# Kernel optimization log

Measured on AMD Instinct MI355X. Metric: run time of the kernel, lower is better.

The kernel has to match this reference:

```python
import math
import jax, jax.numpy as jnp
import numpy as np

B, T, C = 2, 2048, 1024
H, HKV, HD = 16, 4, 64  # n_head, n_kv_head, head_dim
G = H // HKV            # GQA groups
WS = 1024               # sliding window size
GATE_CH = 32


def setup_inputs() -> dict:
    key = jax.random.key(0)
    ks = jax.random.split(key, 8)
    x = jax.random.normal(ks[0], (B, T, C), dtype=jnp.float32)
    ve = jax.random.normal(ks[1], (B, T, HKV * HD), dtype=jnp.float32)
    # realistic RoPE tables: half head_dim frequencies
    d = HD // 2
    inv_freq = 1.0 / (10000.0 ** (jnp.arange(d, dtype=jnp.float32) / d))
    angles = jnp.arange(T, dtype=jnp.float32)[:, None] * inv_freq[None, :]  # (T, d)
    cos = jnp.cos(angles)[None, :, None, :]  # (1, T, 1, d)
    sin = jnp.sin(angles)[None, :, None, :]
    s = 0.02
    Wq = s * jax.random.normal(ks[2], (C, H * HD), dtype=jnp.float32)
    Wk = s * jax.random.normal(ks[3], (C, HKV * HD), dtype=jnp.float32)
    Wv = s * jax.random.normal(ks[4], (C, HKV * HD), dtype=jnp.float32)
    Wproj = s * jax.random.normal(ks[5], (C, C), dtype=jnp.float32)
    Wg = s * jax.random.normal(ks[6], (GATE_CH, HKV), dtype=jnp.float32)
    return {"x": x, "ve": ve, "cos": cos, "sin": sin,
            "Wq": Wq, "Wk": Wk, "Wv": Wv, "Wproj": Wproj, "Wg": Wg, "ws": WS}


def _rope(u, cos, sin):
    d = u.shape[-1] // 2
    u1, u2 = u[..., :d], u[..., d:]
    return jnp.concatenate([u1 * cos + u2 * sin, -u1 * sin + u2 * cos], axis=-1)


def _rmsnorm(u):
    eps = jnp.finfo(u.dtype).eps
    return u * jax.lax.rsqrt(jnp.mean(u * u, axis=-1, keepdims=True) + eps)


def reference(x, ve, cos, sin, Wq, Wk, Wv, Wproj, Wg, ws):
    b, t, c = x.shape
    q = (x @ Wq).reshape(b, t, H, HD)
    k = (x @ Wk).reshape(b, t, HKV, HD)
    v = (x @ Wv).reshape(b, t, HKV, HD)
    # value-embedding gate: 2*sigmoid over first 32 channels of x
    gate = 2.0 * jax.nn.sigmoid(x[..., :GATE_CH] @ Wg)  # (b, t, HKV)
    v = v + gate[..., None] * ve.reshape(b, t, HKV, HD)
    q = _rmsnorm(_rope(q, cos, sin))
    k = _rmsnorm(_rope(k, cos, sin))
    # GQA: view q as (b, t, HKV, G, HD), contract against shared k/v per kv-head
    qg = q.reshape(b, t, HKV, G, HD)
    scale = 1.0 / math.sqrt(HD)
    scores = jnp.einsum('bqhgd,bkhd->bhgqk', qg, k) * scale  # (b, HKV, G, t, t)
    pos = jnp.arange(t)
    # key j attends iff i - ws + 1 <= j <= i (sliding causal window)
    mask = (pos[None, :] >= pos[:, None] - ws + 1) & (pos[None, :] <= pos[:, None])
    scores = jnp.where(mask[None, None, None], scores, -jnp.inf)
    attn = jax.nn.softmax(scores, axis=-1)
    y = jnp.einsum('bhgqk,bkhd->bqhgd', attn, v).reshape(b, t, H * HD)
    return y @ Wproj
```

## Files before the change

kernel.cpp:

```cpp
#include <hip/hip_runtime.h>
#include <hip/hip_bf16.h>

#define Bq 2
#define Tq 2048
#define Cq 1024
#define Hq 16
#define HKVq 4
#define HDq 64
#define Gq 4
#define WSq 1024
#define GATE_CHq 32

typedef __attribute__((ext_vector_type(8))) short short8;
typedef __attribute__((ext_vector_type(4))) float f32x4;
typedef __attribute__((ext_vector_type(2))) unsigned int u32x2;
typedef unsigned int u32;
typedef unsigned short u16;

#if __has_builtin(__builtin_amdgcn_exp2f)
#define EXP2(x) __builtin_amdgcn_exp2f(x)
#else
#define EXP2(x) exp2f(x)
#endif

__device__ __forceinline__ u16 f2bf(float f) {
  u32 u = __float_as_uint(f);
  u32 r = (u + 0x7FFFu + ((u >> 16) & 1u)) >> 16;
  return (u16)r;
}
__device__ __forceinline__ float bf2f(u16 u) {
  return __uint_as_float(((u32)u) << 16);
}

__device__ __forceinline__ void gl_lds16(const u16* g, u16* l) {
  __builtin_amdgcn_global_load_lds(
      (const u32 __attribute__((address_space(1)))*)g,
      (u32 __attribute__((address_space(3)))*)l, 16, 0, 0);
}

__global__ __launch_bounds__(256) void qkv_gemm_fused(
    const u16* __restrict__ A, const u16* __restrict__ Bt,
    const float* __restrict__ ve, const float* __restrict__ cosp,
    const float* __restrict__ sinp, const float* __restrict__ gatebuf,
    u16* __restrict__ Qb, u16* __restrict__ Kb, u16* __restrict__ Vtb) {
  __shared__ __attribute__((aligned(16))) u16 As[64 * 64];
  __shared__ __attribute__((aligned(16))) u16 Bs[128 * 64];

  const int bx = blockIdx.x;
  const int bm0 = blockIdx.y * 64, bn0 = bx * 128;
  const int tid = threadIdx.x;
  const int w = tid >> 6, lane = tid & 63;
  const int wm = (w >> 1) * 32, wn = (w & 1) * 64;
  const int quad = lane >> 4, l16 = lane & 15;
  const int K = 1024;

  f32x4 acc[2][4];
#pragma unroll
  for (int mt = 0; mt < 2; mt++)
#pragma unroll
    for (int nt = 0; nt < 4; nt++) acc[mt][nt] = (f32x4){0.f, 0.f, 0.f, 0.f};

  int goffA[2], goffB[4];
#pragma unroll
  for (int i = 0; i < 2; i++) {
    int s = i * 256 + tid;
    int m = s >> 3, gp = s & 7;
    goffA[i] = m * K + (gp ^ (m & 7)) * 8;
  }
#pragma unroll
  for (int i = 0; i < 4; i++) {
    int s = i * 256 + tid;
    int m = s >> 3, gp = s & 7;
    goffB[i] = m * K + (gp ^ (m & 7)) * 8;
  }
  const u16* Ab = A + (long)bm0 * K;
  const u16* Bb = Bt + (long)bn0 * K;

  for (int k0 = 0; k0 < K; k0 += 64) {
    __syncthreads();
#pragma unroll
    for (int i = 0; i < 2; i++)
      gl_lds16(Ab + goffA[i] + k0, &As[(i * 256 + w * 64) * 8]);
#pragma unroll
    for (int i = 0; i < 4; i++)
      gl_lds16(Bb + goffB[i] + k0, &Bs[(i * 256 + w * 64) * 8]);
    __syncthreads();

#pragma unroll
    for (int ks = 0; ks < 2; ks++) {
      short8 af[2], bf[4];
#pragma unroll
      for (int mt = 0; mt < 2; mt++) {
        int ml = wm + mt * 16 + l16;
        af[mt] = *(const short8*)&As[ml * 64 + (((ks * 4 + quad) ^ (ml & 7)) * 8)];
      }
#pragma unroll
      for (int nt = 0; nt < 4; nt++) {
        int nl = wn + nt * 16 + l16;
        bf[nt] = *(const short8*)&Bs[nl * 64 + (((ks * 4 + quad) ^ (nl & 7)) * 8)];
      }
#pragma unroll
      for (int mt = 0; mt < 2; mt++)
#pragma unroll
        for (int nt = 0; nt < 4; nt++)
          acc[mt][nt] = __builtin_amdgcn_mfma_f32_16x16x32_bf16(
              af[mt], bf[nt], acc[mt][nt], 0, 0, 0);
    }
  }

  const int b = bm0 >> 11;
  const int tseq0 = (bm0 & 2047) + wm;

  if (bx < 10) {
    u16* Dst;
    if (bx < 8) {
      int hh = bx * 2 + (w & 1);
      int hkv = hh >> 2, g = hh & 3;
      Dst = Qb + ((long)((b * 4 + hkv) * 4 + g) * Tq) * 64;
    } else {
      int kk = (bx - 8) * 2 + (w & 1);
      Dst = Kb + ((long)(b * 4 + kk) * Tq) * 64;
    }
#pragma unroll
    for (int mt = 0; mt < 2; mt++) {
#pragma unroll
      for (int r = 0; r < 4; r++) {
        int t = tseq0 + mt * 16 + quad * 4 + r;
        float c0 = cosp[t * 32 + l16];
        float s0 = sinp[t * 32 + l16];
        float c1 = cosp[t * 32 + 16 + l16];
        float s1 = sinp[t * 32 + 16 + l16];
        float a0 = acc[mt][0][r], a1 = acc[mt][1][r];
        float a2 = acc[mt][2][r], a3 = acc[mt][3][r];
        float rp0 = a0 * c0 + a2 * s0;
        float rp1 = a1 * c1 + a3 * s1;
        float rp2 = a2 * c0 - a0 * s0;
        float rp3 = a3 * c1 - a1 * s1;
        float ss = rp0 * rp0 + rp1 * rp1 + rp2 * rp2 + rp3 * rp3;
        ss += __shfl_xor(ss, 1);
        ss += __shfl_xor(ss, 2);
        ss += __shfl_xor(ss, 4);
        ss += __shfl_xor(ss, 8);
        float sc = rsqrtf(ss * (1.f / 64.f) + 1.1920928955078125e-07f);
        u16* drow = Dst + (long)t * 64;
        drow[l16] = f2bf(rp0 * sc);
        drow[16 + l16] = f2bf(rp1 * sc);
        drow[32 + l16] = f2bf(rp2 * sc);
        drow[48 + l16] = f2bf(rp3 * sc);
      }
    }
  } else {
    int kk = (bx - 10) * 2 + (w & 1);
    u16* Dst = Vtb + ((long)(b * 4 + kk) * 64) * Tq;
#pragma unroll
    for (int mt = 0; mt < 2; mt++) {
      float vals[4][4];
#pragma unroll
      for (int r = 0; r < 4; r++) {
        int t = tseq0 + mt * 16 + quad * 4 + r;
        long bt = (long)b * Tq + t;
        float gv = gatebuf[bt * 4 + kk];
        const float* verow = ve + bt * 256 + kk * 64;
#pragma unroll
        for (int nt = 0; nt < 4; nt++)
          vals[nt][r] = acc[mt][nt][r] + gv * verow[nt * 16 + l16];
      }
      int t0m = tseq0 + mt * 16 + quad * 4;
#pragma unroll
      for (int nt = 0; nt < 4; nt++) {
        int d = nt * 16 + l16;
        union { short4 v; u16 u[4]; } p;
#pragma unroll
        for (int r = 0; r < 4; r++) p.u[r] = f2bf(vals[nt][r]);
        *(short4*)(Dst + (long)d * Tq + t0m) = p.v;
      }
    }
  }
}

__global__ __launch_bounds__(256) void gemm_proj(
    const u16* __restrict__ A, const u16* __restrict__ Bt,
    float* __restrict__ C, int M, int N, int K) {
  __shared__ __attribute__((aligned(16))) u16 As[64 * 64];
  __shared__ __attribute__((aligned(16))) u16 Bs[128 * 64];

  const int bm0 = blockIdx.y * 64, bn0 = blockIdx.x * 128;
  const int tid = threadIdx.x;
  const int w = tid >> 6, lane = tid & 63;
  const int wm = (w >> 1) * 32, wn = (w & 1) * 64;
  const int quad = lane >> 4, l16 = lane & 15;

  f32x4 acc[2][4];
#pragma unroll
  for (int mt = 0; mt < 2; mt++)
#pragma unroll
    for (int nt = 0; nt < 4; nt++) acc[mt][nt] = (f32x4){0.f, 0.f, 0.f, 0.f};

  int goffA[2], goffB[4];
#pragma unroll
  for (int i = 0; i < 2; i++) {
    int s = i * 256 + tid;
    int m = s >> 3, gp = s & 7;
    goffA[i] = m * K + (gp ^ (m & 7)) * 8;
  }
#pragma unroll
  for (int i = 0; i < 4; i++) {
    int s = i * 256 + tid;
    int m = s >> 3, gp = s & 7;
    goffB[i] = m * K + (gp ^ (m & 7)) * 8;
  }
  const u16* Ab = A + (long)bm0 * K;
  const u16* Bb = Bt + (long)bn0 * K;

  for (int k0 = 0; k0 < K; k0 += 64) {
    __syncthreads();
#pragma unroll
    for (int i = 0; i < 2; i++)
      gl_lds16(Ab + goffA[i] + k0, &As[(i * 256 + w * 64) * 8]);
#pragma unroll
    for (int i = 0; i < 4; i++)
      gl_lds16(Bb + goffB[i] + k0, &Bs[(i * 256 + w * 64) * 8]);
    __syncthreads();

#pragma unroll
    for (int ks = 0; ks < 2; ks++) {
      short8 af[2], bf[4];
#pragma unroll
      for (int mt = 0; mt < 2; mt++) {
        int ml = wm + mt * 16 + l16;
        af[mt] = *(const short8*)&As[ml * 64 + (((ks * 4 + quad) ^ (ml & 7)) * 8)];
      }
#pragma unroll
      for (int nt = 0; nt < 4; nt++) {
        int nl = wn + nt * 16 + l16;
        bf[nt] = *(const short8*)&Bs[nl * 64 + (((ks * 4 + quad) ^ (nl & 7)) * 8)];
      }
#pragma unroll
      for (int mt = 0; mt < 2; mt++)
#pragma unroll
        for (int nt = 0; nt < 4; nt++)
          acc[mt][nt] = __builtin_amdgcn_mfma_f32_16x16x32_bf16(
              af[mt], bf[nt], acc[mt][nt], 0, 0, 0);
    }
  }

#pragma unroll
  for (int mt = 0; mt < 2; mt++)
#pragma unroll
    for (int nt = 0; nt < 4; nt++) {
      int row0 = bm0 + wm + mt * 16 + quad * 4;
      int col = bn0 + wn + nt * 16 + l16;
#pragma unroll
      for (int r = 0; r < 4; r++)
        C[(long)(row0 + r) * N + col] = acc[mt][nt][r];
    }
}

__global__ __launch_bounds__(256) void prep(
    const float* __restrict__ x, u16* __restrict__ xb,
    const float* __restrict__ Wq, const float* __restrict__ Wk,
    const float* __restrict__ Wv, const float* __restrict__ Wproj,
    const float* __restrict__ Wg, u16* __restrict__ Dqkv,
    u16* __restrict__ Dproj, float* __restrict__ gatebuf) {
  __shared__ float tile[64][65];
  int bx = blockIdx.x;
  int tid = threadIdx.x;
  if (bx < 2048) {
    int i = (bx * 256 + tid) * 8;
    float4 a = *(const float4*)(x + i);
    float4 b = *(const float4*)(x + i + 4);
    union { short8 v; u16 u[8]; } o;
    o.u[0] = f2bf(a.x); o.u[1] = f2bf(a.y); o.u[2] = f2bf(a.z); o.u[3] = f2bf(a.w);
    o.u[4] = f2bf(b.x); o.u[5] = f2bf(b.y); o.u[6] = f2bf(b.z); o.u[7] = f2bf(b.w);
    *(short8*)(xb + i) = o.v;
    return;
  }
  if (bx >= 2688) {
    int p = (bx - 2688) * 256 + tid;
    int bt = p >> 2, kk = p & 3;
    const float* xr = x + (long)bt * Cq;
    float dot = 0.f;
#pragma unroll
    for (int i = 0; i < GATE_CHq; i++) dot += xr[i] * Wg[i * HKVq + kk];
    gatebuf[p] = 2.f / (1.f + expf(-dot));
    return;
  }
  int wb = bx - 2048;
  int obx = wb >> 4;
  int k0 = (wb & 15) * 64;
  const float* S;
  u16* Dst;
  int N, nb;
  if (obx < 16)      { S = Wq;    N = 1024; nb = obx;      Dst = Dqkv; }
  else if (obx < 20) { S = Wk;    N = 256;  nb = obx - 16; Dst = Dqkv + 1024 * 1024; }
  else if (obx < 24) { S = Wv;    N = 256;  nb = obx - 20; Dst = Dqkv + 1280 * 1024; }
  else               { S = Wproj; N = 1024; nb = obx - 24; Dst = Dproj; }
  int n0 = nb * 64;
#pragma unroll
  for (int i = 0; i < 16; i++) {
    int idx = i * 256 + tid;
    int kl = idx >> 6, nl = idx & 63;
    tile[kl][nl] = S[(long)(k0 + kl) * N + n0 + nl];
  }
  __syncthreads();
#pragma unroll
  for (int i = 0; i < 16; i++) {
    int idx = i * 256 + tid;
    int nl = idx >> 6, kl = idx & 63;
    Dst[(long)(n0 + nl) * 1024 + k0 + kl] = f2bf(tile[kl][nl]);
  }
}

#define CEXP 0.18033688011112042f
#define CEXP8 1.4426950408889634f

template <bool MASK>
__device__ __forceinline__ void attn_half(
    int k0h, int key_base, int vg_base, int q0, int quad, int l16,
    const u16* __restrict__ Ks, const u16* __restrict__ Vts,
    u32* __restrict__ myPs, const short8 (&QB)[2][2], f32x4 (&O)[2][4],
    float (&lsum)[2]) {
  f32x4 S4[4][2];
#pragma unroll
  for (int kt4 = 0; kt4 < 4; kt4++) {
    int key = key_base + kt4 * 16 + l16;
    short8 kb0 = *(const short8*)(&Ks[key * 64 + ((quad ^ (key & 7)) * 8)]);
    short8 kb1 = *(const short8*)(&Ks[key * 64 + (((4 + quad) ^ (key & 7)) * 8)]);
#pragma unroll
    for (int qj = 0; qj < 2; qj++) {
      f32x4 acc = (f32x4){0.f, 0.f, 0.f, 0.f};
      acc = __builtin_amdgcn_mfma_f32_16x16x32_bf16(kb0, QB[qj][0], acc, 0, 0, 0);
      acc = __builtin_amdgcn_mfma_f32_16x16x32_bf16(kb1, QB[qj][1], acc, 0, 0, 0);
      S4[kt4][qj] = acc;
    }
  }

#pragma unroll
  for (int kt4 = 0; kt4 < 4; kt4++)
#pragma unroll
    for (int qj = 0; qj < 2; qj++) {
      float Pv[4];
#pragma unroll
      for (int r = 0; r < 4; r++) {
        float sv = S4[kt4][qj][r];
        if (MASK) {
          int kpos = k0h + kt4 * 16 + quad * 4 + r;
          int qpos = q0 + qj * 16 + l16;
          bool valid = (kpos <= qpos) && (kpos >= qpos - (WSq - 1));
          sv = valid ? sv : -1e30f;
        }
        float p = EXP2(__builtin_fmaf(sv, CEXP, -CEXP8));
        Pv[r] = p;
        lsum[qj] += p;
      }
      u32x2 pk;
#pragma unroll
      for (int rp = 0; rp < 2; rp++) {
        u32 lo = __float_as_uint(Pv[2 * rp]) + 0x8000u;
        u32 hi = __float_as_uint(Pv[2 * rp + 1]) + 0x8000u;
        pk[rp] = __builtin_amdgcn_perm(hi, lo, 0x07060302u);
      }
      *(u32x2*)(&myPs[(qj * 16 + l16) * 36 + kt4 * 8 + quad * 2]) = pk;
    }

  short8 vb[4][2];
#pragma unroll
  for (int nt = 0; nt < 4; nt++) {
    int d = nt * 16 + l16;
    vb[nt][0] = *(const short8*)(&Vts[d * 128 + (((vg_base + quad) ^ (d & 7)) * 8)]);
    vb[nt][1] =
        *(const short8*)(&Vts[d * 128 + (((vg_base + 4 + quad) ^ (d & 7)) * 8)]);
  }

#pragma unroll
  for (int qj = 0; qj < 2; qj++) {
    const u32* prow = &myPs[(qj * 16 + l16) * 36];
    short8 pa0 = *(const short8*)(prow + quad * 4);
    short8 pa1 = *(const short8*)(prow + 16 + quad * 4);
#pragma unroll
    for (int nt = 0; nt < 4; nt++) {
      O[qj][nt] =
          __builtin_amdgcn_mfma_f32_16x16x32_bf16(pa0, vb[nt][0], O[qj][nt], 0, 0, 0);
      O[qj][nt] =
          __builtin_amdgcn_mfma_f32_16x16x32_bf16(pa1, vb[nt][1], O[qj][nt], 0, 0, 0);
    }
  }
}

__global__ __launch_bounds__(256, 2) void attn_mfma(
    const u16* __restrict__ Qb, const u16* __restrict__ Kb,
    const u16* __restrict__ Vtb, u16* __restrict__ Yb) {
  __shared__ __attribute__((aligned(16))) u16 Ks[128 * 64];
  __shared__ __attribute__((aligned(16))) u16 Vts[64 * 128];
  __shared__ __attribute__((aligned(16))) u32 Ps[4][2][32 * 36];

  int bid = blockIdx.x;
  int bh = bid & 7;
  int qt32 = bid >> 3;
  int hkv = bh & 3;
  int b = bh >> 2;
  int q0 = qt32 * 32;
  int tid = threadIdx.x;
  int g = tid >> 6;
  int lane = tid & 63;
  int quad = lane >> 4;
  int l16 = lane & 15;

  short8 QB[2][2];
#pragma unroll
  for (int qj = 0; qj < 2; qj++) {
    const u16* qb =
        Qb + ((long)((bh * 4 + g) * Tq + q0 + qj * 16 + l16)) * 64 + quad * 8;
    QB[qj][0] = *(const short8*)(qb);
    QB[qj][1] = *(const short8*)(qb + 32);
  }

  f32x4 O[2][4];
#pragma unroll
  for (int qj = 0; qj < 2; qj++)
#pragma unroll
    for (int nt = 0; nt < 4; nt++) O[qj][nt] = (f32x4){0.f, 0.f, 0.f, 0.f};
  float lsum[2] = {0.f, 0.f};

  int lo = q0 - (WSq - 1);
  int st = (lo < 0 ? 0 : lo) >> 7;
  int et = (q0 + 31) >> 7;

  const u16* Kbase = Kb + ((long)bh * Tq) * 64;
  const u16* Vbase = Vtb + ((long)bh * 64) * Tq;

  int rowoffK[4], rowoffV[4];
#pragma unroll
  for (int i = 0; i < 4; i++) {
    int s = i * 256 + tid;
    int kr = s >> 3, kgp = s & 7;
    rowoffK[i] = kr * 64 + (kgp ^ (kr & 7)) * 8;
    int d = s >> 4, vgp = s & 15;
    rowoffV[i] = d * Tq + (vgp ^ (d & 7)) * 8;
  }

  for (int kt = st; kt <= et; kt++) {
    int k0 = kt << 7;
    __syncthreads();
#pragma unroll
    for (int i = 0; i < 4; i++) {
      gl_lds16(Kbase + (long)k0 * 64 + rowoffK[i], &Ks[(i * 256 + g * 64) * 8]);
      gl_lds16(Vbase + k0 + rowoffV[i], &Vts[(i * 256 + g * 64) * 8]);
    }
    __syncthreads();

    bool needC = (k0 + 127 > q0);
    bool needW = (k0 < q0 - 992);
    if (needC || needW) {
      attn_half<true>(k0, 0, 0, q0, quad, l16, Ks, Vts, &Ps[g][0][0], QB, O, lsum);
      attn_half<true>(k0 + 64, 64, 8, q0, quad, l16, Ks, Vts, &Ps[g][1][0], QB,
                      O, lsum);
    } else {
      attn_half<false>(k0, 0, 0, q0, quad, l16, Ks, Vts, &Ps[g][0][0], QB, O,
                       lsum);
      attn_half<false>(k0 + 64, 64, 8, q0, quad, l16, Ks, Vts, &Ps[g][1][0], QB,
                       O, lsum);
    }
  }

#pragma unroll
  for (int qj = 0; qj < 2; qj++) {
    lsum[qj] += __shfl_xor(lsum[qj], 16);
    lsum[qj] += __shfl_xor(lsum[qj], 32);
  }

  int h = hkv * 4 + g;
#pragma unroll
  for (int qj = 0; qj < 2; qj++) {
    float invl[4];
#pragma unroll
    for (int r = 0; r < 4; r++) invl[r] = 1.f / __shfl(lsum[qj], quad * 4 + r);
#pragma unroll
    for (int nt = 0; nt < 4; nt++)
#pragma unroll
      for (int r = 0; r < 4; r++)
        Yb[((long)(b * Tq + q0 + qj * 16 + quad * 4 + r)) * 1024 + h * 64 +
           nt * 16 + l16] = f2bf(O[qj][nt][r] * invl[r]);
  }
}

extern "C" void kernel_launch(void* const* d_in, const int* in_sizes, int n_in,
                              void* d_out, int out_size, void* d_ws,
                              size_t ws_size, hipStream_t stream) {
  const float* x     = (const float*)d_in[0];
  const float* ve    = (const float*)d_in[1];
  const float* cosp  = (const float*)d_in[2];
  const float* sinp  = (const float*)d_in[3];
  const float* Wq    = (const float*)d_in[4];
  const float* Wk    = (const float*)d_in[5];
  const float* Wv    = (const float*)d_in[6];
  const float* Wproj = (const float*)d_in[7];
  const float* Wg    = (const float*)d_in[8];

  char* base = (char*)d_ws;
  u16* xb      = (u16*)(base);
  u16* Yb      = xb;
  u16* WqkvT   = (u16*)(base + 8388608);
  u16* WprojT  = (u16*)(base + 11534336);
  u16* Qb      = (u16*)(base + 13631488);
  u16* Kb      = (u16*)(base + 22020096);
  u16* Vtb     = (u16*)(base + 24117248);
  float* gateb = (float*)(base + 26214400);
  float* out = (float*)d_out;

  prep<<<2752, 256, 0, stream>>>(x, xb, Wq, Wk, Wv, Wproj, Wg, WqkvT, WprojT,
                                 gateb);
  qkv_gemm_fused<<<dim3(12, 64), 256, 0, stream>>>(xb, WqkvT, ve, cosp, sinp,
                                                   gateb, Qb, Kb, Vtb);
  attn_mfma<<<512, 256, 0, stream>>>(Qb, Kb, Vtb, Yb);
  gemm_proj<<<dim3(8, 64), 256, 0, stream>>>(Yb, WprojT, out, 4096, 1024, 1024);
}
```

Before: 162.2 us.

## Load K/V fragments directly from global memory, drop shared K/V staging

```diff
diff --git a/kernel.cpp b/kernel.cpp
--- a/kernel.cpp
+++ b/kernel.cpp
@@ -315,25 +315,35 @@
 #define CEXP8 1.4426950408889634f
 
 template <bool MASK>
-__device__ __forceinline__ void attn_half(
-    int k0h, int key_base, int vg_base, int q0, int quad, int l16,
-    const u16* __restrict__ Ks, const u16* __restrict__ Vts,
-    u32* __restrict__ myPs, const short8 (&QB)[2][2], f32x4 (&O)[2][4],
-    float (&lsum)[2]) {
+__device__ __forceinline__ void attn_chunk(
+    int k0, int q0, int quad, int l16, const u16* __restrict__ kf_addr,
+    const u16* __restrict__ vf_addr, u32* __restrict__ myPs,
+    const short8 (&QB)[2][2], f32x4 (&O)[2][4], float (&lsum)[2]) {
+  short8 kf[4][2];
+#pragma unroll
+  for (int kt4 = 0; kt4 < 4; kt4++) {
+    kf[kt4][0] = *(const short8*)(kf_addr + kt4 * 1024);
+    kf[kt4][1] = *(const short8*)(kf_addr + kt4 * 1024 + 32);
+  }
+  short8 vf[4][2];
+#pragma unroll
+  for (int nt = 0; nt < 4; nt++) {
+    vf[nt][0] = *(const short8*)(vf_addr + (long)nt * 16 * Tq);
+    vf[nt][1] = *(const short8*)(vf_addr + (long)nt * 16 * Tq + 32);
+  }
+
   f32x4 S4[4][2];
 #pragma unroll
-  for (int kt4 = 0; kt4 < 4; kt4++) {
-    int key = key_base + kt4 * 16 + l16;
-    short8 kb0 = *(const short8*)(&Ks[key * 64 + ((quad ^ (key & 7)) * 8)]);
-    short8 kb1 = *(const short8*)(&Ks[key * 64 + (((4 + quad) ^ (key & 7)) * 8)]);
+  for (int kt4 = 0; kt4 < 4; kt4++)
 #pragma unroll
     for (int qj = 0; qj < 2; qj++) {
       f32x4 acc = (f32x4){0.f, 0.f, 0.f, 0.f};
-      acc = __builtin_amdgcn_mfma_f32_16x16x32_bf16(kb0, QB[qj][0], acc, 0, 0, 0);
-      acc = __builtin_amdgcn_mfma_f32_16x16x32_bf16(kb1, QB[qj][1], acc, 0, 0, 0);
+      acc = __builtin_amdgcn_mfma_f32_16x16x32_bf16(kf[kt4][0], QB[qj][0], acc,
+                                                    0, 0, 0);
+      acc = __builtin_amdgcn_mfma_f32_16x16x32_bf16(kf[kt4][1], QB[qj][1], acc,
+                                                    0, 0, 0);
       S4[kt4][qj] = acc;
     }
-  }
 
 #pragma unroll
   for (int kt4 = 0; kt4 < 4; kt4++)
@@ -344,7 +354,7 @@
       for (int r = 0; r < 4; r++) {
         float sv = S4[kt4][qj][r];
         if (MASK) {
-          int kpos = k0h + kt4 * 16 + quad * 4 + r;
+          int kpos = k0 + kt4 * 16 + quad * 4 + r;
           int qpos = q0 + qj * 16 + l16;
           bool valid = (kpos <= qpos) && (kpos >= qpos - (WSq - 1));
           sv = valid ? sv : -1e30f;
@@ -363,15 +373,6 @@
       *(u32x2*)(&myPs[(qj * 16 + l16) * 36 + kt4 * 8 + quad * 2]) = pk;
     }
 
-  short8 vb[4][2];
-#pragma unroll
-  for (int nt = 0; nt < 4; nt++) {
-    int d = nt * 16 + l16;
-    vb[nt][0] = *(const short8*)(&Vts[d * 128 + (((vg_base + quad) ^ (d & 7)) * 8)]);
-    vb[nt][1] =
-        *(const short8*)(&Vts[d * 128 + (((vg_base + 4 + quad) ^ (d & 7)) * 8)]);
-  }
-
 #pragma unroll
   for (int qj = 0; qj < 2; qj++) {
     const u32* prow = &myPs[(qj * 16 + l16) * 36];
@@ -380,19 +381,17 @@
 #pragma unroll
     for (int nt = 0; nt < 4; nt++) {
       O[qj][nt] =
-          __builtin_amdgcn_mfma_f32_16x16x32_bf16(pa0, vb[nt][0], O[qj][nt], 0, 0, 0);
+          __builtin_amdgcn_mfma_f32_16x16x32_bf16(pa0, vf[nt][0], O[qj][nt], 0, 0, 0);
       O[qj][nt] =
-          __builtin_amdgcn_mfma_f32_16x16x32_bf16(pa1, vb[nt][1], O[qj][nt], 0, 0, 0);
-    }
-  }
-}
-
-__global__ __launch_bounds__(256, 2) void attn_mfma(
+          __builtin_amdgcn_mfma_f32_16x16x32_bf16(pa1, vf[nt][1], O[qj][nt], 0, 0, 0);
+    }
+  }
+}
+
+__global__ __launch_bounds__(256, 3) void attn_mfma(
     const u16* __restrict__ Qb, const u16* __restrict__ Kb,
     const u16* __restrict__ Vtb, u16* __restrict__ Yb) {
-  __shared__ __attribute__((aligned(16))) u16 Ks[128 * 64];
-  __shared__ __attribute__((aligned(16))) u16 Vts[64 * 128];
-  __shared__ __attribute__((aligned(16))) u32 Ps[4][2][32 * 36];
+  __shared__ __attribute__((aligned(16))) u32 Ps[4][32 * 36];
 
   int bid = blockIdx.x;
   int bh = bid & 7;
@@ -423,45 +422,29 @@
   float lsum[2] = {0.f, 0.f};
 
   int lo = q0 - (WSq - 1);
-  int st = (lo < 0 ? 0 : lo) >> 7;
-  int et = (q0 + 31) >> 7;
+  int k0s = (lo < 0 ? 0 : lo) & ~63;
+  int k0e = q0 & ~63;
 
   const u16* Kbase = Kb + ((long)bh * Tq) * 64;
   const u16* Vbase = Vtb + ((long)bh * 64) * Tq;
-
-  int rowoffK[4], rowoffV[4];
-#pragma unroll
-  for (int i = 0; i < 4; i++) {
-    int s = i * 256 + tid;
-    int kr = s >> 3, kgp = s & 7;
-    rowoffK[i] = kr * 64 + (kgp ^ (kr & 7)) * 8;
-    int d = s >> 4, vgp = s & 15;
-    rowoffV[i] = d * Tq + (vgp ^ (d & 7)) * 8;
-  }
-
-  for (int kt = st; kt <= et; kt++) {
-    int k0 = kt << 7;
-    __syncthreads();
-#pragma unroll
-    for (int i = 0; i < 4; i++) {
-      gl_lds16(Kbase + (long)k0 * 64 + rowoffK[i], &Ks[(i * 256 + g * 64) * 8]);
-      gl_lds16(Vbase + k0 + rowoffV[i], &Vts[(i * 256 + g * 64) * 8]);
-    }
-    __syncthreads();
-
-    bool needC = (k0 + 127 > q0);
-    bool needW = (k0 < q0 - 992);
-    if (needC || needW) {
-      attn_half<true>(k0, 0, 0, q0, quad, l16, Ks, Vts, &Ps[g][0][0], QB, O, lsum);
-      attn_half<true>(k0 + 64, 64, 8, q0, quad, l16, Ks, Vts, &Ps[g][1][0], QB,
-                      O, lsum);
-    } else {
-      attn_half<false>(k0, 0, 0, q0, quad, l16, Ks, Vts, &Ps[g][0][0], QB, O,
-                       lsum);
-      attn_half<false>(k0 + 64, 64, 8, q0, quad, l16, Ks, Vts, &Ps[g][1][0], QB,
-                       O, lsum);
-    }
-  }
+  u32* myPs = &Ps[g][0];
+
+  const u16* kf_addr = Kbase + (long)(k0s + l16) * 64 + quad * 8;
+  const u16* vf_addr = Vbase + (long)l16 * Tq + k0s + quad * 8;
+
+  int k0 = k0s;
+  if (q0 >= WSq && k0 < k0e) {
+    attn_chunk<true>(k0, q0, quad, l16, kf_addr, vf_addr, myPs, QB, O, lsum);
+    k0 += 64;
+    kf_addr += 64 * 64;
+    vf_addr += 64;
+  }
+  for (; k0 < k0e; k0 += 64) {
+    attn_chunk<false>(k0, q0, quad, l16, kf_addr, vf_addr, myPs, QB, O, lsum);
+    kf_addr += 64 * 64;
+    vf_addr += 64;
+  }
+  attn_chunk<true>(k0, q0, quad, l16, kf_addr, vf_addr, myPs, QB, O, lsum);
 
 #pragma unroll
   for (int qj = 0; qj < 2; qj++) {
```

Result: slower. 193.6 us (+19.4%).
